# Optimization experiments

Measured on AMD Instinct MI355X. Metric: run time of the kernel, lower is better.

## Reference

```python
import jax, jax.numpy as jnp
import numpy as np

B, S, D = 4, 2048, 1024
H = 4 * D          # expert hidden dim
E_SPEC = 4         # num specific experts
E_SHR = 2          # num shared experts
TOP_K = 2


def setup_inputs() -> dict:
    key = jax.random.key(0)
    ks = jax.random.split(key, 16)
    s = 0.02
    return {
        "x": jax.random.normal(ks[0], (B, S, D), jnp.float32),
        # specific experts (stacked over expert axis)
        "spec_w1": jax.random.normal(ks[1], (E_SPEC, D, H), jnp.float32) * s,
        "spec_b1": jnp.zeros((E_SPEC, H), jnp.float32),
        "spec_w2": jax.random.normal(ks[2], (E_SPEC, H, D), jnp.float32) * s,
        "spec_b2": jnp.zeros((E_SPEC, D), jnp.float32),
        "spec_rw": jax.random.normal(ks[3], (D, E_SPEC), jnp.float32) * s,
        "spec_rb": jnp.zeros((E_SPEC,), jnp.float32),
        # shared experts
        "shr_w1": jax.random.normal(ks[4], (E_SHR, D, H), jnp.float32) * s,
        "shr_b1": jnp.zeros((E_SHR, H), jnp.float32),
        "shr_w2": jax.random.normal(ks[5], (E_SHR, H, D), jnp.float32) * s,
        "shr_b2": jnp.zeros((E_SHR, D), jnp.float32),
        "shr_rw": jax.random.normal(ks[6], (D, E_SHR), jnp.float32) * s,
        "shr_rb": jnp.zeros((E_SHR,), jnp.float32),
    }


def _expert_mlp(xf, w1, b1, w2, b2):
    # xf: [T, D]; w1: [E, D, H]; w2: [E, H, D] -> [E, T, D]
    h = jax.nn.gelu(jnp.einsum("td,edh->eth", xf, w1) + b1[:, None, :],
                    approximate=False)
    return jnp.einsum("eth,ehd->etd", h, w2) + b2[:, None, :]


def reference(x, spec_w1, spec_b1, spec_w2, spec_b2, spec_rw, spec_rb,
              shr_w1, shr_b1, shr_w2, shr_b2, shr_rw, shr_rb):
    b, s, d = x.shape
    xf = x.reshape(-1, d)                      # [T, D]
    T = xf.shape[0]

    # --- specific (top-k) routing ---
    spec_probs = jax.nn.softmax(xf @ spec_rw + spec_rb, axis=-1)   # [T, E]
    topk_probs, topk_idx = jax.lax.top_k(spec_probs, TOP_K)        # [T, K]

    # aux load-balancing loss
    counts = jnp.zeros((E_SPEC,), jnp.float32).at[topk_idx.reshape(-1)].add(1.0)
    fraction = counts / (T * TOP_K)
    aux_loss = E_SPEC * jnp.sum(fraction * spec_probs.mean(axis=0))

    # gate[t, e] = sum_k topk_probs[t,k] * 1[topk_idx[t,k]==e]
    gate = jnp.sum(jax.nn.one_hot(topk_idx, E_SPEC, dtype=xf.dtype)
                   * topk_probs[..., None], axis=1)                # [T, E]

    spec_out_e = _expert_mlp(xf, spec_w1, spec_b1, spec_w2, spec_b2)  # [E, T, D]
    specific_out = jnp.einsum("te,etd->td", gate, spec_out_e)

    # --- shared (dense) experts ---
    shr_probs = jax.nn.softmax(xf @ shr_rw + shr_rb, axis=-1)      # [T, E_shr]
    shr_out_e = _expert_mlp(xf, shr_w1, shr_b1, shr_w2, shr_b2)    # [E_shr, T, D]
    shared_out = jnp.einsum("te,etd->td", shr_probs, shr_out_e)

    final = (specific_out + shared_out).reshape(b, s, d)
    return final, aux_loss
```

## Files before the change

### kernel.cpp

```cpp
#include <hip/hip_runtime.h>
#include <hip/hip_bf16.h>

#define T_TOK 8192
#define DDIM 1024
#define HDIM 4096

typedef __bf16 bf16;
typedef bf16 bf16x8 __attribute__((ext_vector_type(8)));
typedef float f32x4 __attribute__((ext_vector_type(4)));

#define ASM_VMCNT(n) asm volatile("s_waitcnt vmcnt(" #n ")" ::: "memory")
#define MFMA16(a, b, c) __builtin_amdgcn_mfma_f32_16x16x32_bf16((a), (b), (c), 0, 0, 0)

__device__ __forceinline__ void gl_lds16(const void* g, void* l) {
  __builtin_amdgcn_global_load_lds(
      (const __attribute__((address_space(1))) unsigned int*)g,
      (__attribute__((address_space(3))) unsigned int*)l, 16, 0, 0);
}

__device__ __forceinline__ float gelu_f(float v) {
  const float x = v * 0.7071067811865475f;
  const float ax = fabsf(x);
  const float t = 1.0f / fmaf(0.3275911f, ax, 1.0f);
  float p = fmaf(1.061405429f, t, -1.453152027f);
  p = fmaf(p, t, 1.421413741f);
  p = fmaf(p, t, -0.284496736f);
  p = fmaf(p, t, 0.254829592f);
  p = p * t;
  const float e = __expf(-ax * ax);
  const float er = fmaf(-p, e, 1.0f);
  const float erfx = (x >= 0.0f) ? er : -er;
  return 0.5f * v * (1.0f + erfx);
}

__global__ __launch_bounds__(256) void convert_x(const float* __restrict__ x,
                                                 bf16* __restrict__ xb) {
  const size_t i = ((size_t)blockIdx.x * 256 + threadIdx.x) * 8;
  const float4 v0 = *(const float4*)(x + i);
  const float4 v1 = *(const float4*)(x + i + 4);
  bf16x8 o;
  o[0] = (bf16)v0.x; o[1] = (bf16)v0.y; o[2] = (bf16)v0.z; o[3] = (bf16)v0.w;
  o[4] = (bf16)v1.x; o[5] = (bf16)v1.y; o[6] = (bf16)v1.z; o[7] = (bf16)v1.w;
  *(bf16x8*)(xb + i) = o;
}

__global__ __launch_bounds__(256) void transpose_convert(
    const float* __restrict__ src, bf16* __restrict__ dst, int R, int C) {
  __shared__ float tile[32][33];
  const size_t mat = (size_t)blockIdx.z * R * C;
  const int c0 = blockIdx.x * 32, r0 = blockIdx.y * 32;
  const int tx = threadIdx.x & 31, ty = threadIdx.x >> 5;
#pragma unroll
  for (int i = 0; i < 4; ++i)
    tile[ty + 8 * i][tx] =
        src[mat + (size_t)(r0 + ty + 8 * i) * C + c0 + tx];
  __syncthreads();
#pragma unroll
  for (int i = 0; i < 4; ++i)
    dst[mat + (size_t)(c0 + ty + 8 * i) * R + r0 + tx] =
        (bf16)tile[tx][ty + 8 * i];
}

__global__ __launch_bounds__(256) void router_probs(
    const float* __restrict__ x, const float* __restrict__ srw,
    const float* __restrict__ srb, const float* __restrict__ hrw,
    const float* __restrict__ hrb, float* __restrict__ gate,
    float4* __restrict__ probs4, int* __restrict__ top2) {
  const int lane = threadIdx.x & 63;
  const int w = threadIdx.x >> 6;
  const int t = blockIdx.x * 4 + w;

  const float* xr = x + (size_t)t * DDIM;
  float p0 = 0, p1 = 0, p2 = 0, p3 = 0, p4 = 0, p5 = 0;
#pragma unroll
  for (int c = 0; c < 4; ++c) {
    const int d = c * 256 + lane * 4;
    const float4 xv = *(const float4*)(xr + d);
    const float xa[4] = {xv.x, xv.y, xv.z, xv.w};
#pragma unroll
    for (int j = 0; j < 4; ++j) {
      const float xd = xa[j];
      const float4 r4 = *(const float4*)(srw + (size_t)(d + j) * 4);
      p0 += xd * r4.x; p1 += xd * r4.y; p2 += xd * r4.z; p3 += xd * r4.w;
      const float2 r2 = *(const float2*)(hrw + (size_t)(d + j) * 2);
      p4 += xd * r2.x; p5 += xd * r2.y;
    }
  }
#pragma unroll
  for (int off = 32; off >= 1; off >>= 1) {
    p0 += __shfl_xor(p0, off);
    p1 += __shfl_xor(p1, off);
    p2 += __shfl_xor(p2, off);
    p3 += __shfl_xor(p3, off);
    p4 += __shfl_xor(p4, off);
    p5 += __shfl_xor(p5, off);
  }
  if (lane == 0) {
    const float l0 = p0 + srb[0], l1 = p1 + srb[1];
    const float l2 = p2 + srb[2], l3 = p3 + srb[3];
    const float m = fmaxf(fmaxf(l0, l1), fmaxf(l2, l3));
    const float e0 = expf(l0 - m), e1 = expf(l1 - m);
    const float e2 = expf(l2 - m), e3 = expf(l3 - m);
    const float s = e0 + e1 + e2 + e3;
    float pr[4] = {e0 / s, e1 / s, e2 / s, e3 / s};
    int i1 = 0; float v1 = pr[0];
#pragma unroll
    for (int e = 1; e < 4; ++e) if (pr[e] > v1) { v1 = pr[e]; i1 = e; }
    int i2 = -1; float v2 = -1.0f;
#pragma unroll
    for (int e = 0; e < 4; ++e)
      if (e != i1 && pr[e] > v2) { v2 = pr[e]; i2 = e; }
    float g[4] = {0, 0, 0, 0};
    g[i1] = v1; g[i2] = v2;
    float* gr = gate + (size_t)t * 8;
    gr[0] = g[0]; gr[1] = g[1]; gr[2] = g[2]; gr[3] = g[3];
    const float h0 = p4 + hrb[0], h1 = p5 + hrb[1];
    const float mh = fmaxf(h0, h1);
    const float q0 = expf(h0 - mh), q1 = expf(h1 - mh);
    const float qs = q0 + q1;
    gr[4] = q0 / qs; gr[5] = q1 / qs; gr[6] = 0; gr[7] = 0;
    probs4[t] = make_float4(pr[0], pr[1], pr[2], pr[3]);
    top2[t] = i1 | (i2 << 8);
  }
}

__global__ __launch_bounds__(1024) void scan_build(
    const int* __restrict__ top2, const float4* __restrict__ probs4,
    int* __restrict__ cnt, int* __restrict__ lists, float* __restrict__ auxg) {
  __shared__ unsigned long long sc[1024];
  __shared__ float4 rp[512];
  const int tid = threadIdx.x;

  int ee[8];
  unsigned long long c = 0;
  float4 ps = make_float4(0.f, 0.f, 0.f, 0.f);
#pragma unroll
  for (int j = 0; j < 8; ++j) {
    const int t = tid * 8 + j;
    const int p = top2[t];
    ee[j] = p;
    const int a = p & 15, b = (p >> 8) & 15;
    c += (1ULL << (16 * a)) + (1ULL << (16 * b));
    const float4 pv = probs4[t];
    ps.x += pv.x; ps.y += pv.y; ps.z += pv.z; ps.w += pv.w;
  }
  sc[tid] = c;
  __syncthreads();
  for (int off = 1; off < 1024; off <<= 1) {
    const unsigned long long mine = sc[tid];
    const unsigned long long prev = (tid >= off) ? sc[tid - off] : 0ULL;
    __syncthreads();
    sc[tid] = mine + prev;
    __syncthreads();
  }
  const unsigned long long incl = sc[tid];
  const unsigned long long tot = sc[1023];
  const unsigned long long excl = incl - c;
  int q0 = (int)(excl & 0xffff), q1 = (int)((excl >> 16) & 0xffff);
  int q2 = (int)((excl >> 32) & 0xffff), q3 = (int)((excl >> 48) & 0xffff);
#pragma unroll
  for (int j = 0; j < 8; ++j) {
    const int t = tid * 8 + j;
    const int a = ee[j] & 15, b = (ee[j] >> 8) & 15;
    const int pa = (a == 0) ? q0 : (a == 1) ? q1 : (a == 2) ? q2 : q3;
    lists[a * 8192 + pa] = t;
    q0 += (a == 0); q1 += (a == 1); q2 += (a == 2); q3 += (a == 3);
    const int pb = (b == 0) ? q0 : (b == 1) ? q1 : (b == 2) ? q2 : q3;
    lists[b * 8192 + pb] = t;
    q0 += (b == 0); q1 += (b == 1); q2 += (b == 2); q3 += (b == 3);
  }
  if (tid == 1023) {
    const int c0 = (int)(tot & 0xffff), c1 = (int)((tot >> 16) & 0xffff);
    const int c2 = (int)((tot >> 32) & 0xffff), c3 = (int)((tot >> 48) & 0xffff);
    cnt[0] = c0; cnt[1] = c1; cnt[2] = c2; cnt[3] = c3;
    auxg[0] = (float)c0; auxg[1] = (float)c1;
    auxg[2] = (float)c2; auxg[3] = (float)c3;
  }
  if (tid >= 512) rp[tid - 512] = ps;
  __syncthreads();
  if (tid < 512) {
    const float4 o = rp[tid];
    ps.x += o.x; ps.y += o.y; ps.z += o.z; ps.w += o.w;
  }
  for (int w = 256; w >= 1; w >>= 1) {
    __syncthreads();
    if (tid >= w && tid < 2 * w) rp[tid - w] = ps;
    __syncthreads();
    if (tid < w) {
      const float4 o = rp[tid];
      ps.x += o.x; ps.y += o.y; ps.z += o.z; ps.w += o.w;
    }
  }
  if (tid == 0) {
    auxg[4] = ps.x; auxg[5] = ps.y; auxg[6] = ps.z; auxg[7] = ps.w;
  }
}

__global__ void aux_finalize(const float* __restrict__ auxg,
                             float* __restrict__ outp) {
  float a = 0.0f;
#pragma unroll
  for (int e = 0; e < 4; ++e)
    a += (auxg[e] / (float)(T_TOK * 2)) * (auxg[4 + e] / (float)T_TOK);
  outp[0] = 4.0f * a;
}

template <int MODE>
__global__ __launch_bounds__(256, 3) void gemmv(
    const bf16* __restrict__ A, const bf16* __restrict__ B, int N, int K,
    const float* __restrict__ bias, bf16* __restrict__ Hout, int NBn,
    int CH_M, int CH_N, const int* __restrict__ cnt,
    const int* __restrict__ lists, int eid) {
  __shared__ __align__(1024) bf16 As[3 * 128 * 32];
  __shared__ __align__(1024) bf16 Bs[3 * 128 * 32];

  const int tid = threadIdx.x;
  const int lane = tid & 63, wid = tid >> 6;
  const int wm = wid >> 1, wn = wid & 1;
  const int lr = lane & 15, lg = lane >> 4;

  int bm, bn;
  if constexpr (MODE == 4) {
    const int nbm = ((cnt[eid] + 127) & ~127) >> 7;
    const int CHm = (nbm + 3) >> 2;
    const int need = 8 * CHm * CH_N;
    if (blockIdx.x >= need) return;
    const int xc = blockIdx.x & 7;
    const int idx = blockIdx.x >> 3;
    bm = (xc >> 1) * CHm + idx / CH_N;
    bn = (xc & 1) * CH_N + idx % CH_N;
    if (bm >= nbm) return;
  } else {
    const int xcd = blockIdx.x & 7;
    const int idx = blockIdx.x >> 3;
    const int ncn = NBn / CH_N;
    bm = (xcd / ncn) * CH_M + idx / CH_N;
    bn = (xcd % ncn) * CH_N + idx % CH_N;
  }

  const int rl = tid >> 2;
  const int c = ((tid & 3) * 16) ^ (((rl >> 1) & 3) << 4);
  int ar0 = bm * 128 + rl, ar1 = ar0 + 64;
  if constexpr (MODE == 4) {
    const int* lp = lists + eid * 8192;
    int t = lp[ar0]; ar0 = t < 0 ? 0 : t;
    t = lp[ar1]; ar1 = t < 0 ? 0 : t;
  }
  const bf16* sA0 = A + (size_t)ar0 * K + (c >> 1);
  const bf16* sA1 = A + (size_t)ar1 * K + (c >> 1);
  const bf16* sB0 = B + (size_t)(bn * 128 + rl) * K + (c >> 1);
  const bf16* sB1 = B + (size_t)(bn * 128 + 64 + rl) * K + (c >> 1);
  char* const dA0 = (char*)As + wid * 1024;
  char* const dA1 = (char*)As + 4096 + wid * 1024;
  char* const dB0 = (char*)Bs + wid * 1024;
  char* const dB1 = (char*)Bs + 4096 + wid * 1024;

  const int rkey = ((lr >> 1) & 3) << 4;
  const char* Ard = (const char*)As + (wm * 64 + lr) * 64 + ((lg * 16) ^ rkey);
  const char* Brd = (const char*)Bs + (wn * 64 + lr) * 64 + ((lg * 16) ^ rkey);

  f32x4 acc[4][4] = {};
  const int NT = K >> 5;

#define GV_STAGE(KO, SLOT)                    \
  gl_lds16(sA0 + (KO), dA0 + (SLOT)*8192);    \
  gl_lds16(sA1 + (KO), dA1 + (SLOT)*8192);    \
  gl_lds16(sB0 + (KO), dB0 + (SLOT)*8192);    \
  gl_lds16(sB1 + (KO), dB1 + (SLOT)*8192);
  GV_STAGE(0, 0)
  GV_STAGE(32, 1)
  GV_STAGE(64, 2)
  ASM_VMCNT(8);
  __builtin_amdgcn_s_barrier();

#define GV_ITER(KT, SLOT)                                                  \
  {                                                                        \
    bf16x8 af[4], bfr[4];                                                  \
    _Pragma("unroll") for (int mf = 0; mf < 4; ++mf)                       \
        af[mf] = *(const bf16x8*)(Ard + (SLOT)*8192 + mf * 1024);          \
    _Pragma("unroll") for (int nf = 0; nf < 4; ++nf)                       \
        bfr[nf] = *(const bf16x8*)(Brd + (SLOT)*8192 + nf * 1024);         \
    asm volatile("s_waitcnt lgkmcnt(0)" ::: "memory");                     \
    __builtin_amdgcn_s_setprio(1);                                         \
    _Pragma("unroll") for (int mf = 0; mf < 4; ++mf)                       \
        _Pragma("unroll") for (int nf = 0; nf < 4; ++nf)                   \
            acc[mf][nf] = MFMA16(af[mf], bfr[nf], acc[mf][nf]);            \
    __builtin_amdgcn_s_setprio(0);                                         \
    __builtin_amdgcn_s_barrier();                                          \
    if ((KT) + 3 < NT) {                                                   \
      const int ko_ = ((KT) + 3) << 5;                                     \
      GV_STAGE(ko_, SLOT)                                                  \
      ASM_VMCNT(8);                                                        \
    } else if ((KT) + 2 < NT) {                                            \
      ASM_VMCNT(4);                                                        \
    } else if ((KT) + 1 < NT) {                                            \
      ASM_VMCNT(0);                                                        \
    }                                                                      \
    __builtin_amdgcn_s_barrier();                                          \
  }

  for (int kt0 = 0; kt0 < NT; kt0 += 3) {
    GV_ITER(kt0, 0)
    if (kt0 + 1 < NT) GV_ITER(kt0 + 1, 1)
    if (kt0 + 2 < NT) GV_ITER(kt0 + 2, 2)
  }

  const int colb = bn * 128 + wn * 64;
  const int rowb = bm * 128 + wm * 64 + lg * 4;
  float bv[4];
#pragma unroll
  for (int nf = 0; nf < 4; ++nf) bv[nf] = bias[colb + nf * 16 + lr];
#pragma unroll
  for (int mf = 0; mf < 4; ++mf)
#pragma unroll
    for (int nf = 0; nf < 4; ++nf) {
      const int col = colb + nf * 16 + lr;
#pragma unroll
      for (int r = 0; r < 4; ++r) {
        const int row = rowb + mf * 16 + r;
        Hout[(size_t)row * N + col] = (bf16)gelu_f(acc[mf][nf][r] + bv[nf]);
      }
    }
}

template <int BN_, int MODE>
__global__ __launch_bounds__(512, 2) void gemm4p(
    const bf16* __restrict__ A, const bf16* __restrict__ B, int M, int N,
    int K, const float* __restrict__ bias, bf16* __restrict__ Hout,
    float* __restrict__ Fout, const float* __restrict__ gate, int gidx,
    int NBn, int CH_M, int CH_N, const int* __restrict__ cnt,
    const int* __restrict__ lists, int eid) {
  constexpr int NREP = BN_ / 64;
  constexpr int NHF = NREP / 2;
  constexpr int WNT = BN_ / 4;
  constexpr int ABYTES = 256 * 64 * 2;
  constexpr int BBYTES = BN_ * 64 * 2;
  constexpr bool DYN = (MODE == 3);

  __shared__ __align__(1024) bf16 Alds[2 * 256 * 64];
  __shared__ __align__(1024) bf16 Blds[2 * BN_ * 64];

  const int tid = threadIdx.x;
  const int lane = tid & 63, wid = tid >> 6;
  const int wm = wid >> 2, wn = wid & 3;
  const int lr = lane & 15, lg = lane >> 4;

  int bm, bn;
  if constexpr (DYN) {
    const int nbm = ((cnt[eid] + 255) & ~255) >> 8;
    const int CHm = (nbm + 3) >> 2;
    constexpr int CHn = (BN_ == 256) ? 8 : 4;
    const int need = 8 * CHm * CHn;
    if (blockIdx.x >= need) return;
    const int xc = blockIdx.x & 7;
    const int idx = blockIdx.x >> 3;
    bm = (xc >> 1) * CHm + idx / CHn;
    bn = (xc & 1) * CHn + idx % CHn;
    if (bm >= nbm) return;
  } else {
    const int xcd = blockIdx.x & 7;
    const int idx = blockIdx.x >> 3;
    const int ncn = NBn / CH_N;
    bm = (xcd / ncn) * CH_M + idx / CH_N;
    bn = (xcd % ncn) * CH_N + idx % CH_N;
  }

  const int NT = K >> 6;

  const int L = tid * 16;
  const int rl = L >> 7;
  const int colb = (L & 127) ^ ((rl & 7) << 4);

  const int ar0 = bm * 256 + rl;
  const bf16* sAc0 = A + (size_t)ar0 * K + (colb >> 1);
  const bf16* sAc1 = A + (size_t)(ar0 + 64) * K + (colb >> 1);
  const bf16* sAc2 = A + (size_t)(ar0 + 128) * K + (colb >> 1);
  const bf16* sAc3 = A + (size_t)(ar0 + 192) * K + (colb >> 1);
  const bf16* sB = B + (size_t)(bn * BN_ + rl) * K + (colb >> 1);

  char* const ldsA = (char*)Alds;
  char* const ldsB = (char*)Blds;
  const int wb = wid * 1024;
  char* const stA[2] = {ldsA + wb, ldsA + ABYTES + wb};
  char* const stB[2] = {ldsB + wb, ldsB + BBYTES + wb};

  const int ax0 = (lg * 16) ^ ((lr & 7) << 4);
  const int ax1 = ax0 ^ 64;
  const int aro = (wm * 128 + lr) * 128;
  const int bro = (wn * WNT + lr) * 128;
  const char* const Ak0[2] = {ldsA + aro + ax0, ldsA + ABYTES + aro + ax0};
  const char* const Ak1[2] = {ldsA + aro + ax1, ldsA + ABYTES + aro + ax1};
  const char* const Bk0[2] = {ldsB + bro + ax0, ldsB + BBYTES + bro + ax0};
  const char* const Bk1[2] = {ldsB + bro + ax1, ldsB + BBYTES + bro + ax1};

  f32x4 acc[8][NREP] = {};

  gl_lds16(sAc0, stA[0]);
  gl_lds16(sAc1, stA[0] + 8192);
  gl_lds16(sAc2, stA[0] + 16384);
  gl_lds16(sAc3, stA[0] + 24576);
  gl_lds16(sB, stB[0]);
  gl_lds16(sB + (size_t)64 * K, stB[0] + 8192);
  if constexpr (BN_ == 256) {
    gl_lds16(sB + (size_t)128 * K, stB[0] + 16384);
    gl_lds16(sB + (size_t)192 * K, stB[0] + 24576);
  }
  gl_lds16(sB + 64, stB[1]);
  gl_lds16(sB + (size_t)64 * K + 64, stB[1] + 8192);
  if constexpr (BN_ == 256) {
    gl_lds16(sB + (size_t)128 * K + 64, stB[1] + 16384);
    gl_lds16(sB + (size_t)192 * K + 64, stB[1] + 24576);
  }
  gl_lds16(sAc0 + 64, stA[1]);
  gl_lds16(sAc1 + 64, stA[1] + 8192);
  if constexpr (BN_ == 256) ASM_VMCNT(6); else ASM_VMCNT(4);
  __builtin_amdgcn_s_barrier();

  for (int kt0 = 0; kt0 < NT; kt0 += 2) {
#pragma unroll
    for (int par = 0; par < 2; ++par) {
      const int kt = kt0 + par;
      const int cur = par, oth = par ^ 1;
      const bool st1 = (kt + 1) < NT, st2 = (kt + 2) < NT;
      const size_t ko1 = (size_t)(kt + 1) << 6, ko2 = (size_t)(kt + 2) << 6;
      const char* Ac0 = Ak0[cur]; const char* Ac1 = Ak1[cur];
      const char* Bc0 = Bk0[cur]; const char* Bc1 = Bk1[cur];

      bf16x8 af[4][2], bfr[NREP][2];

#pragma unroll
      for (int mf = 0; mf < 4; ++mf) {
        af[mf][0] = *(const bf16x8*)(Ac0 + mf * 2048);
        af[mf][1] = *(const bf16x8*)(Ac1 + mf * 2048);
      }
#pragma unroll
      for (int nf = 0; nf < NHF; ++nf) {
        bfr[nf][0] = *(const bf16x8*)(Bc0 + nf * 2048);
        bfr[nf][1] = *(const bf16x8*)(Bc1 + nf * 2048);
      }
      if (st1) {
        gl_lds16(sAc2 + ko1, stA[oth] + 16384);
        gl_lds16(sAc3 + ko1, stA[oth] + 24576);
      }
      __builtin_amdgcn_s_barrier();
      asm volatile("s_waitcnt lgkmcnt(0)" ::: "memory");
      __builtin_amdgcn_sched_barrier(0);
      __builtin_amdgcn_s_setprio(1);
#pragma unroll
      for (int mf = 0; mf < 4; ++mf)
#pragma unroll
        for (int nf = 0; nf < NHF; ++nf) {
          acc[mf][nf] = MFMA16(af[mf][0], bfr[nf][0], acc[mf][nf]);
          acc[mf][nf] = MFMA16(af[mf][1], bfr[nf][1], acc[mf][nf]);
        }
      __builtin_amdgcn_s_setprio(0);
      __builtin_amdgcn_s_barrier();

#pragma unroll
      for (int nf = NHF; nf < NREP; ++nf) {
        bfr[nf][0] = *(const bf16x8*)(Bc0 + nf * 2048);
        bfr[nf][1] = *(const bf16x8*)(Bc1 + nf * 2048);
      }
      __builtin_amdgcn_s_barrier();
      asm volatile("s_waitcnt lgkmcnt(0)" ::: "memory");
      __builtin_amdgcn_sched_barrier(0);
      __builtin_amdgcn_s_setprio(1);
#pragma unroll
      for (int mf = 0; mf < 4; ++mf)
#pragma unroll
        for (int nf = NHF; nf < NREP; ++nf) {
          acc[mf][nf] = MFMA16(af[mf][0], bfr[nf][0], acc[mf][nf]);
          acc[mf][nf] = MFMA16(af[mf][1], bfr[nf][1], acc[mf][nf]);
        }
      __builtin_amdgcn_s_setprio(0);
      __builtin_amdgcn_s_barrier();

#pragma unroll
      for (int mf = 0; mf < 4; ++mf) {
        af[mf][0] = *(const bf16x8*)(Ac0 + 8192 + mf * 2048);
        af[mf][1] = *(const bf16x8*)(Ac1 + 8192 + mf * 2048);
      }
      if (st2) {
        gl_lds16(sB + ko2, stB[cur]);
        gl_lds16(sB + (size_t)64 * K + ko2, stB[cur] + 8192);
      }
      __builtin_amdgcn_s_barrier();
      asm volatile("s_waitcnt lgkmcnt(0)" ::: "memory");
      __builtin_amdgcn_sched_barrier(0);
      __builtin_amdgcn_s_setprio(1);
#pragma unroll
      for (int mf = 0; mf < 4; ++mf)
#pragma unroll
        for (int nf = 0; nf < NHF; ++nf) {
          acc[4 + mf][nf] = MFMA16(af[mf][0], bfr[nf][0], acc[4 + mf][nf]);
          acc[4 + mf][nf] = MFMA16(af[mf][1], bfr[nf][1], acc[4 + mf][nf]);
        }
      __builtin_amdgcn_s_setprio(0);
      __builtin_amdgcn_s_barrier();

      if (st2) {
        if constexpr (BN_ == 256) {
          gl_lds16(sB + (size_t)128 * K + ko2, stB[cur] + 16384);
          gl_lds16(sB + (size_t)192 * K + ko2, stB[cur] + 24576);
        }
        gl_lds16(sAc0 + ko2, stA[cur]);
        gl_lds16(sAc1 + ko2, stA[cur] + 8192);
      }
      __builtin_amdgcn_s_setprio(1);
#pragma unroll
      for (int mf = 0; mf < 4; ++mf)
#pragma unroll
        for (int nf = NHF; nf < NREP; ++nf) {
          acc[4 + mf][nf] = MFMA16(af[mf][0], bfr[nf][0], acc[4 + mf][nf]);
          acc[4 + mf][nf] = MFMA16(af[mf][1], bfr[nf][1], acc[4 + mf][nf]);
        }
      __builtin_amdgcn_s_setprio(0);
      if (st2) {
        if constexpr (BN_ == 256) ASM_VMCNT(6); else ASM_VMCNT(4);
        __builtin_amdgcn_s_barrier();
      } else if (st1) {
        ASM_VMCNT(0);
        __builtin_amdgcn_s_barrier();
      }
    }
  }

  const int colb2 = bn * BN_ + wn * WNT;
  const int rowb = bm * 256 + wm * 128 + lg * 4;
  float bv[NREP];
#pragma unroll
  for (int nf = 0; nf < NREP; ++nf) bv[nf] = bias[colb2 + nf * 16 + lr];
#pragma unroll
  for (int mf = 0; mf < 8; ++mf) {
    if constexpr (MODE == 1 || MODE == 2) {
      float gv[4];
#pragma unroll
      for (int r = 0; r < 4; ++r)
        gv[r] = gate[(size_t)(rowb + mf * 16 + r) * 8 + gidx];
#pragma unroll
      for (int nf = 0; nf < NREP; ++nf) {
        const int col = colb2 + nf * 16 + lr;
#pragma unroll
        for (int r = 0; r < 4; ++r) {
          const float v = acc[mf][nf][r] + bv[nf];
          const size_t oi = (size_t)(rowb + mf * 16 + r) * N + col;
          if constexpr (MODE == 1)
            Fout[oi] += gv[r] * v;
          else
            Fout[oi] = gv[r] * v;
        }
      }
    } else {
      const int* lp = lists + eid * 8192;
      int tok[4]; float gv[4];
#pragma unroll
      for (int r = 0; r < 4; ++r) {
        tok[r] = lp[rowb + mf * 16 + r];
        gv[r] = tok[r] >= 0 ? gate[(size_t)tok[r] * 8 + gidx] : 0.0f;
      }
#pragma unroll
      for (int nf = 0; nf < NREP; ++nf) {
        const int col = colb2 + nf * 16 + lr;
#pragma unroll
        for (int r = 0; r < 4; ++r) {
          if (tok[r] >= 0) {
            const float v = acc[mf][nf][r] + bv[nf];
            Fout[(size_t)tok[r] * N + col] += gv[r] * v;
          }
        }
      }
    }
  }
}

extern "C" void kernel_launch(void* const* d_in, const int* in_sizes, int n_in,
                              void* d_out, int out_size, void* d_ws,
                              size_t ws_size, hipStream_t stream) {
  const float* x = (const float*)d_in[0];
  const float* spec_w1 = (const float*)d_in[1];
  const float* spec_b1 = (const float*)d_in[2];
  const float* spec_w2 = (const float*)d_in[3];
  const float* spec_b2 = (const float*)d_in[4];
  const float* spec_rw = (const float*)d_in[5];
  const float* spec_rb = (const float*)d_in[6];
  const float* shr_w1 = (const float*)d_in[7];
  const float* shr_b1 = (const float*)d_in[8];
  const float* shr_w2 = (const float*)d_in[9];
  const float* shr_b2 = (const float*)d_in[10];
  const float* shr_rw = (const float*)d_in[11];
  const float* shr_rb = (const float*)d_in[12];
  float* out = (float*)d_out;

  char* ws = (char*)d_ws;
  const size_t OFF_W1 = 16777216;
  const size_t OFF_W2 = OFF_W1 + 50331648;
  const size_t OFF_H = OFF_W2 + 50331648;
  const size_t OFF_GATE = OFF_H + 67108864;
  const size_t OFF_AUX = OFF_GATE + 262144;
  const size_t OFF_CNT = OFF_AUX + 64;
  const size_t OFF_LIST = OFF_CNT + 64;
  const size_t OFF_T2 = OFF_LIST + 131072;
  const size_t OFF_P4 = OFF_T2 + 32768;
  bf16* xb = (bf16*)ws;
  bf16* w1t = (bf16*)(ws + OFF_W1);
  bf16* w2t = (bf16*)(ws + OFF_W2);
  bf16* hbuf = (bf16*)(ws + OFF_H);
  float* gate = (float*)(ws + OFF_GATE);
  float* auxg = (float*)(ws + OFF_AUX);
  int* cnt = (int*)(ws + OFF_CNT);
  int* lists = (int*)(ws + OFF_LIST);
  int* top2 = (int*)(ws + OFF_T2);
  float4* probs4 = (float4*)(ws + OFF_P4);

  hipMemsetAsync(lists, 0xFF, 4 * 8192 * 4, stream);

  convert_x<<<(T_TOK * DDIM) / 2048, 256, 0, stream>>>(x, xb);
  transpose_convert<<<dim3(HDIM / 32, DDIM / 32, 4), 256, 0, stream>>>(
      spec_w1, w1t, DDIM, HDIM);
  transpose_convert<<<dim3(HDIM / 32, DDIM / 32, 2), 256, 0, stream>>>(
      shr_w1, w1t + (size_t)4 * DDIM * HDIM, DDIM, HDIM);
  transpose_convert<<<dim3(DDIM / 32, HDIM / 32, 4), 256, 0, stream>>>(
      spec_w2, w2t, HDIM, DDIM);
  transpose_convert<<<dim3(DDIM / 32, HDIM / 32, 2), 256, 0, stream>>>(
      shr_w2, w2t + (size_t)4 * DDIM * HDIM, HDIM, DDIM);

  router_probs<<<T_TOK / 4, 256, 0, stream>>>(x, spec_rw, spec_rb, shr_rw,
                                              shr_rb, gate, probs4, top2);
  scan_build<<<1, 1024, 0, stream>>>(top2, probs4, cnt, lists, auxg);

  for (int es = 0; es < 2; ++es) {
    const bf16* w1e = w1t + (size_t)(4 + es) * DDIM * HDIM;
    const bf16* w2e = w2t + (size_t)(4 + es) * DDIM * HDIM;
    const float* b1e = shr_b1 + (size_t)es * HDIM;
    const float* b2e = shr_b2 + (size_t)es * DDIM;
    gemmv<0><<<2048, 256, 0, stream>>>(xb, w1e, HDIM, DDIM, b1e, hbuf,
                                       32, 16, 16, nullptr, nullptr, 0);
    if (es == 0)
      gemm4p<128, 2><<<256, 512, 0, stream>>>(
          hbuf, w2e, T_TOK, DDIM, HDIM, b2e, nullptr, out, gate, 4,
          8, 8, 4, nullptr, nullptr, 0);
    else
      gemm4p<128, 1><<<256, 512, 0, stream>>>(
          hbuf, w2e, T_TOK, DDIM, HDIM, b2e, nullptr, out, gate, 5,
          8, 8, 4, nullptr, nullptr, 0);
  }

  for (int e = 0; e < 4; ++e) {
    const bf16* w1e = w1t + (size_t)e * DDIM * HDIM;
    const bf16* w2e = w2t + (size_t)e * DDIM * HDIM;
    const float* b1e = spec_b1 + (size_t)e * HDIM;
    const float* b2e = spec_b2 + (size_t)e * DDIM;
    gemmv<4><<<2048, 256, 0, stream>>>(xb, w1e, HDIM, DDIM, b1e, hbuf,
                                       32, 0, 16, cnt, lists, e);
    gemm4p<128, 3><<<256, 512, 0, stream>>>(
        hbuf, w2e, T_TOK, DDIM, HDIM, b2e, nullptr, out, gate, e,
        8, 0, 0, cnt, lists, e);
  }
  aux_finalize<<<1, 1, 0, stream>>>(auxg, out + (size_t)T_TOK * DDIM);
}
```

Before: 1.045 ms.

## Enlarge first-layer GEMM tile to 256 rows and fuse x conversion into router

The first-layer expert GEMM now uses a 256x128 block tile (each wave computes 128x64) instead of 128x128. This doubles the accumulators per thread and halves the grid, with the aim of raising arithmetic intensity and cutting B-operand reloads. Occupancy drops from 3 to 2 blocks per CU, and padding waste grows for routed experts with small token counts. Separately, the fp32-to-bf16 conversion of x is folded into the router kernel so x is read once, removing a separate launch.

```diff
diff --git a/kernel.cpp b/kernel.cpp
--- a/kernel.cpp
+++ b/kernel.cpp
@@ -33,49 +33,25 @@
   return 0.5f * v * (1.0f + erfx);
 }
 
-__global__ __launch_bounds__(256) void convert_x(const float* __restrict__ x,
-                                                 bf16* __restrict__ xb) {
-  const size_t i = ((size_t)blockIdx.x * 256 + threadIdx.x) * 8;
-  const float4 v0 = *(const float4*)(x + i);
-  const float4 v1 = *(const float4*)(x + i + 4);
-  bf16x8 o;
-  o[0] = (bf16)v0.x; o[1] = (bf16)v0.y; o[2] = (bf16)v0.z; o[3] = (bf16)v0.w;
-  o[4] = (bf16)v1.x; o[5] = (bf16)v1.y; o[6] = (bf16)v1.z; o[7] = (bf16)v1.w;
-  *(bf16x8*)(xb + i) = o;
-}
-
-__global__ __launch_bounds__(256) void transpose_convert(
-    const float* __restrict__ src, bf16* __restrict__ dst, int R, int C) {
-  __shared__ float tile[32][33];
-  const size_t mat = (size_t)blockIdx.z * R * C;
-  const int c0 = blockIdx.x * 32, r0 = blockIdx.y * 32;
-  const int tx = threadIdx.x & 31, ty = threadIdx.x >> 5;
-#pragma unroll
-  for (int i = 0; i < 4; ++i)
-    tile[ty + 8 * i][tx] =
-        src[mat + (size_t)(r0 + ty + 8 * i) * C + c0 + tx];
-  __syncthreads();
-#pragma unroll
-  for (int i = 0; i < 4; ++i)
-    dst[mat + (size_t)(c0 + ty + 8 * i) * R + r0 + tx] =
-        (bf16)tile[tx][ty + 8 * i];
-}
-
-__global__ __launch_bounds__(256) void router_probs(
-    const float* __restrict__ x, const float* __restrict__ srw,
-    const float* __restrict__ srb, const float* __restrict__ hrw,
-    const float* __restrict__ hrb, float* __restrict__ gate,
-    float4* __restrict__ probs4, int* __restrict__ top2) {
+__global__ __launch_bounds__(256) void conv_router(
+    const float* __restrict__ x, bf16* __restrict__ xb,
+    const float* __restrict__ srw, const float* __restrict__ srb,
+    const float* __restrict__ hrw, const float* __restrict__ hrb,
+    float* __restrict__ gate, float4* __restrict__ probs4,
+    int* __restrict__ top2) {
   const int lane = threadIdx.x & 63;
   const int w = threadIdx.x >> 6;
   const int t = blockIdx.x * 4 + w;
 
   const float* xr = x + (size_t)t * DDIM;
+  bf16* xbr = xb + (size_t)t * DDIM;
   float p0 = 0, p1 = 0, p2 = 0, p3 = 0, p4 = 0, p5 = 0;
 #pragma unroll
   for (int c = 0; c < 4; ++c) {
     const int d = c * 256 + lane * 4;
     const float4 xv = *(const float4*)(xr + d);
+    bf16 ov[4] = {(bf16)xv.x, (bf16)xv.y, (bf16)xv.z, (bf16)xv.w};
+    *(float2*)(xbr + d) = *(float2*)ov;
     const float xa[4] = {xv.x, xv.y, xv.z, xv.w};
 #pragma unroll
     for (int j = 0; j < 4; ++j) {
@@ -124,6 +100,23 @@
   }
 }
 
+__global__ __launch_bounds__(256) void transpose_convert(
+    const float* __restrict__ src, bf16* __restrict__ dst, int R, int C) {
+  __shared__ float tile[32][33];
+  const size_t mat = (size_t)blockIdx.z * R * C;
+  const int c0 = blockIdx.x * 32, r0 = blockIdx.y * 32;
+  const int tx = threadIdx.x & 31, ty = threadIdx.x >> 5;
+#pragma unroll
+  for (int i = 0; i < 4; ++i)
+    tile[ty + 8 * i][tx] =
+        src[mat + (size_t)(r0 + ty + 8 * i) * C + c0 + tx];
+  __syncthreads();
+#pragma unroll
+  for (int i = 0; i < 4; ++i)
+    dst[mat + (size_t)(c0 + ty + 8 * i) * R + r0 + tx] =
+        (bf16)tile[tx][ty + 8 * i];
+}
+
 __global__ __launch_bounds__(1024) void scan_build(
     const int* __restrict__ top2, const float4* __restrict__ probs4,
     int* __restrict__ cnt, int* __restrict__ lists, float* __restrict__ auxg) {
@@ -206,12 +199,12 @@
 }
 
 template <int MODE>
-__global__ __launch_bounds__(256, 3) void gemmv(
+__global__ __launch_bounds__(256, 2) void gemmw(
     const bf16* __restrict__ A, const bf16* __restrict__ B, int N, int K,
     const float* __restrict__ bias, bf16* __restrict__ Hout, int NBn,
     int CH_M, int CH_N, const int* __restrict__ cnt,
     const int* __restrict__ lists, int eid) {
-  __shared__ __align__(1024) bf16 As[3 * 128 * 32];
+  __shared__ __align__(1024) bf16 As[3 * 256 * 32];
   __shared__ __align__(1024) bf16 Bs[3 * 128 * 32];
 
   const int tid = threadIdx.x;
@@ -221,7 +214,7 @@
 
   int bm, bn;
   if constexpr (MODE == 4) {
-    const int nbm = ((cnt[eid] + 127) & ~127) >> 7;
+    const int nbm = ((cnt[eid] + 255) & ~255) >> 8;
     const int CHm = (nbm + 3) >> 2;
     const int need = 8 * CHm * CH_N;
     if (blockIdx.x >= need) return;
@@ -240,59 +233,65 @@
 
   const int rl = tid >> 2;
   const int c = ((tid & 3) * 16) ^ (((rl >> 1) & 3) << 4);
-  int ar0 = bm * 128 + rl, ar1 = ar0 + 64;
+  int ar0 = bm * 256 + rl, ar1 = ar0 + 64, ar2 = ar0 + 128, ar3 = ar0 + 192;
   if constexpr (MODE == 4) {
     const int* lp = lists + eid * 8192;
-    int t = lp[ar0]; ar0 = t < 0 ? 0 : t;
+    int t;
+    t = lp[ar0]; ar0 = t < 0 ? 0 : t;
     t = lp[ar1]; ar1 = t < 0 ? 0 : t;
+    t = lp[ar2]; ar2 = t < 0 ? 0 : t;
+    t = lp[ar3]; ar3 = t < 0 ? 0 : t;
   }
   const bf16* sA0 = A + (size_t)ar0 * K + (c >> 1);
   const bf16* sA1 = A + (size_t)ar1 * K + (c >> 1);
+  const bf16* sA2 = A + (size_t)ar2 * K + (c >> 1);
+  const bf16* sA3 = A + (size_t)ar3 * K + (c >> 1);
   const bf16* sB0 = B + (size_t)(bn * 128 + rl) * K + (c >> 1);
   const bf16* sB1 = B + (size_t)(bn * 128 + 64 + rl) * K + (c >> 1);
-  char* const dA0 = (char*)As + wid * 1024;
-  char* const dA1 = (char*)As + 4096 + wid * 1024;
-  char* const dB0 = (char*)Bs + wid * 1024;
-  char* const dB1 = (char*)Bs + 4096 + wid * 1024;
+
+  char* const dA = (char*)As + wid * 1024;
+  char* const dB = (char*)Bs + wid * 1024;
 
   const int rkey = ((lr >> 1) & 3) << 4;
-  const char* Ard = (const char*)As + (wm * 64 + lr) * 64 + ((lg * 16) ^ rkey);
+  const char* Ard = (const char*)As + (wm * 128 + lr) * 64 + ((lg * 16) ^ rkey);
   const char* Brd = (const char*)Bs + (wn * 64 + lr) * 64 + ((lg * 16) ^ rkey);
 
-  f32x4 acc[4][4] = {};
+  f32x4 acc[8][4] = {};
   const int NT = K >> 5;
 
-#define GV_STAGE(KO, SLOT)                    \
-  gl_lds16(sA0 + (KO), dA0 + (SLOT)*8192);    \
-  gl_lds16(sA1 + (KO), dA1 + (SLOT)*8192);    \
-  gl_lds16(sB0 + (KO), dB0 + (SLOT)*8192);    \
-  gl_lds16(sB1 + (KO), dB1 + (SLOT)*8192);
-  GV_STAGE(0, 0)
-  GV_STAGE(32, 1)
-  GV_STAGE(64, 2)
-  ASM_VMCNT(8);
+#define GW_STAGE(KO, SLOT)                         \
+  gl_lds16(sA0 + (KO), dA + (SLOT)*16384);         \
+  gl_lds16(sA1 + (KO), dA + (SLOT)*16384 + 4096);  \
+  gl_lds16(sA2 + (KO), dA + (SLOT)*16384 + 8192);  \
+  gl_lds16(sA3 + (KO), dA + (SLOT)*16384 + 12288); \
+  gl_lds16(sB0 + (KO), dB + (SLOT)*8192);          \
+  gl_lds16(sB1 + (KO), dB + (SLOT)*8192 + 4096);
+  GW_STAGE(0, 0)
+  GW_STAGE(32, 1)
+  GW_STAGE(64, 2)
+  ASM_VMCNT(12);
   __builtin_amdgcn_s_barrier();
 
-#define GV_ITER(KT, SLOT)                                                  \
+#define GW_ITER(KT, SLOT)                                                  \
   {                                                                        \
-    bf16x8 af[4], bfr[4];                                                  \
-    _Pragma("unroll") for (int mf = 0; mf < 4; ++mf)                       \
-        af[mf] = *(const bf16x8*)(Ard + (SLOT)*8192 + mf * 1024);          \
+    bf16x8 af[8], bfr[4];                                                  \
+    _Pragma("unroll") for (int mf = 0; mf < 8; ++mf)                       \
+        af[mf] = *(const bf16x8*)(Ard + (SLOT)*16384 + mf * 1024);         \
     _Pragma("unroll") for (int nf = 0; nf < 4; ++nf)                       \
         bfr[nf] = *(const bf16x8*)(Brd + (SLOT)*8192 + nf * 1024);         \
     asm volatile("s_waitcnt lgkmcnt(0)" ::: "memory");                     \
     __builtin_amdgcn_s_setprio(1);                                         \
-    _Pragma("unroll") for (int mf = 0; mf < 4; ++mf)                       \
+    _Pragma("unroll") for (int mf = 0; mf < 8; ++mf)                       \
         _Pragma("unroll") for (int nf = 0; nf < 4; ++nf)                   \
             acc[mf][nf] = MFMA16(af[mf], bfr[nf], acc[mf][nf]);            \
     __builtin_amdgcn_s_setprio(0);                                         \
     __builtin_amdgcn_s_barrier();                                          \
     if ((KT) + 3 < NT) {                                                   \
       const int ko_ = ((KT) + 3) << 5;                                     \
-      GV_STAGE(ko_, SLOT)                                                  \
-      ASM_VMCNT(8);                                                        \
+      GW_STAGE(ko_, SLOT)                                                  \
+      ASM_VMCNT(12);                                                       \
     } else if ((KT) + 2 < NT) {                                            \
-      ASM_VMCNT(4);                                                        \
+      ASM_VMCNT(6);                                                        \
     } else if ((KT) + 1 < NT) {                                            \
       ASM_VMCNT(0);                                                        \
     }                                                                      \
@@ -300,18 +299,18 @@
   }
 
   for (int kt0 = 0; kt0 < NT; kt0 += 3) {
-    GV_ITER(kt0, 0)
-    if (kt0 + 1 < NT) GV_ITER(kt0 + 1, 1)
-    if (kt0 + 2 < NT) GV_ITER(kt0 + 2, 2)
+    GW_ITER(kt0, 0)
+    if (kt0 + 1 < NT) GW_ITER(kt0 + 1, 1)
+    if (kt0 + 2 < NT) GW_ITER(kt0 + 2, 2)
   }
 
   const int colb = bn * 128 + wn * 64;
-  const int rowb = bm * 128 + wm * 64 + lg * 4;
+  const int rowb = bm * 256 + wm * 128 + lg * 4;
   float bv[4];
 #pragma unroll
   for (int nf = 0; nf < 4; ++nf) bv[nf] = bias[colb + nf * 16 + lr];
 #pragma unroll
-  for (int mf = 0; mf < 4; ++mf)
+  for (int mf = 0; mf < 8; ++mf)
 #pragma unroll
     for (int nf = 0; nf < 4; ++nf) {
       const int col = colb + nf * 16 + lr;
@@ -614,7 +613,10 @@
 
   hipMemsetAsync(lists, 0xFF, 4 * 8192 * 4, stream);
 
-  convert_x<<<(T_TOK * DDIM) / 2048, 256, 0, stream>>>(x, xb);
+  conv_router<<<T_TOK / 4, 256, 0, stream>>>(x, xb, spec_rw, spec_rb, shr_rw,
+                                             shr_rb, gate, probs4, top2);
+  scan_build<<<1, 1024, 0, stream>>>(top2, probs4, cnt, lists, auxg);
+
   transpose_convert<<<dim3(HDIM / 32, DDIM / 32, 4), 256, 0, stream>>>(
       spec_w1, w1t, DDIM, HDIM);
   transpose_convert<<<dim3(HDIM / 32, DDIM / 32, 2), 256, 0, stream>>>(
@@ -624,17 +626,13 @@
   transpose_convert<<<dim3(DDIM / 32, HDIM / 32, 2), 256, 0, stream>>>(
       shr_w2, w2t + (size_t)4 * DDIM * HDIM, HDIM, DDIM);
 
-  router_probs<<<T_TOK / 4, 256, 0, stream>>>(x, spec_rw, spec_rb, shr_rw,
-                                              shr_rb, gate, probs4, top2);
-  scan_build<<<1, 1024, 0, stream>>>(top2, probs4, cnt, lists, auxg);
-
   for (int es = 0; es < 2; ++es) {
     const bf16* w1e = w1t + (size_t)(4 + es) * DDIM * HDIM;
     const bf16* w2e = w2t + (size_t)(4 + es) * DDIM * HDIM;
     const float* b1e = shr_b1 + (size_t)es * HDIM;
     const float* b2e = shr_b2 + (size_t)es * DDIM;
-    gemmv<0><<<2048, 256, 0, stream>>>(xb, w1e, HDIM, DDIM, b1e, hbuf,
-                                       32, 16, 16, nullptr, nullptr, 0);
+    gemmw<0><<<1024, 256, 0, stream>>>(xb, w1e, HDIM, DDIM, b1e, hbuf,
+                                       32, 8, 16, nullptr, nullptr, 0);
     if (es == 0)
       gemm4p<128, 2><<<256, 512, 0, stream>>>(
           hbuf, w2e, T_TOK, DDIM, HDIM, b2e, nullptr, out, gate, 4,
@@ -650,7 +648,7 @@
     const bf16* w2e = w2t + (size_t)e * DDIM * HDIM;
     const float* b1e = spec_b1 + (size_t)e * HDIM;
     const float* b2e = spec_b2 + (size_t)e * DDIM;
-    gemmv<4><<<2048, 256, 0, stream>>>(xb, w1e, HDIM, DDIM, b1e, hbuf,
+    gemmw<4><<<1024, 256, 0, stream>>>(xb, w1e, HDIM, DDIM, b1e, hbuf,
                                        32, 0, 16, cnt, lists, e);
     gemm4p<128, 3><<<256, 512, 0, stream>>>(
         hbuf, w2e, T_TOK, DDIM, HDIM, b2e, nullptr, out, gate, e,
```

Measured after the change: 1.054 ms. About the same (+0.8%).
